# Kernel tuning notes

Measured on AMD Instinct MI355X. Metric: run time of the kernel, lower is better.

The kernel has to match this reference:

```python
import jax, jax.numpy as jnp
import numpy as np

EMB = 1024
HEADS = 16
HEAD_DIM = EMB // HEADS
ROPE_BASE = 10000.0


def rotate_half(x):
    # Interleaved rotate: pairs (x0,x1,x2,x3,...) -> (-x1,x0,-x3,x2,...)
    x1 = x[..., ::2]
    x2 = x[..., 1::2]
    return jnp.stack((-x2, x1), axis=-1).reshape(x.shape)


def rope_cos_sin(seq_len, head_dim):
    inv_freq = 1.0 / (ROPE_BASE ** (jnp.arange(0, head_dim, 2, dtype=jnp.float32) / head_dim))
    pos = jnp.arange(seq_len, dtype=jnp.float32)
    freqs = jnp.outer(pos, inv_freq)            # [S, hd/2]
    emb = jnp.concatenate([freqs, freqs], -1)   # [S, hd]  (NOTE: concat, matching source)
    return jnp.cos(emb)[None, None], jnp.sin(emb)[None, None]  # [1,1,S,hd]


def setup_inputs() -> dict:
    key = jax.random.key(0)
    ks = jax.random.split(key, 5)
    B, S = 2, 2048
    x = jax.random.normal(ks[0], (B, S, EMB), dtype=jnp.float32)
    scale = EMB ** -0.5
    Wq = jax.random.normal(ks[1], (EMB, EMB), dtype=jnp.float32) * scale
    Wk = jax.random.normal(ks[2], (EMB, EMB), dtype=jnp.float32) * scale
    Wv = jax.random.normal(ks[3], (EMB, EMB), dtype=jnp.float32) * scale
    Wo = jax.random.normal(ks[4], (EMB, EMB), dtype=jnp.float32) * scale
    return {"x": x, "Wq": Wq, "Wk": Wk, "Wv": Wv, "Wo": Wo}


def reference(x, Wq, Wk, Wv, Wo):
    B, S, E = x.shape
    def shape_heads(t):
        return t.reshape(B, S, HEADS, HEAD_DIM).transpose(0, 2, 1, 3)  # [B,H,S,hd]
    q = shape_heads(x @ Wq.T)
    k = shape_heads(x @ Wk.T)
    v = shape_heads(x @ Wv.T)
    cos, sin = rope_cos_sin(S, HEAD_DIM)
    q = q * cos + rotate_half(q) * sin
    k = k * cos + rotate_half(k) * sin
    scale = HEAD_DIM ** -0.5
    scores = jnp.einsum('bhqd,bhkd->bhqk', q, k) * scale  # [B,H,S,S]
    causal = jnp.triu(jnp.ones((S, S), dtype=bool), k=1)
    scores = jnp.where(causal, -jnp.inf, scores)
    attn = jax.nn.softmax(scores, axis=-1)
    out = jnp.einsum('bhqk,bhkd->bhqd', attn, v)           # [B,H,S,hd]
    out = out.transpose(0, 2, 1, 3).reshape(B, S, E)
    return out @ Wo.T
```

## Files before the change

### kernel.cpp

```cpp
#include <hip/hip_runtime.h>
#include <cstdint>
#include <cstddef>

typedef __bf16 bf16;
typedef __attribute__((ext_vector_type(8))) __bf16 bf16x8;
typedef __attribute__((ext_vector_type(4))) __bf16 bf16x4;
typedef __attribute__((ext_vector_type(4))) float f32x4;

constexpr int kS = 2048;
constexpr int kH = 16;
constexpr int kD = 64;

__device__ __forceinline__ void gload16(const bf16* g, bf16* l) {
  __builtin_amdgcn_global_load_lds((const __attribute__((address_space(1))) void*)g,
                                   (__attribute__((address_space(3))) void*)l, 16, 0, 0);
}

__global__ __launch_bounds__(256) void cast_all_kernel(
    const float* __restrict__ x, const float* __restrict__ wq, const float* __restrict__ wk,
    const float* __restrict__ wv, const float* __restrict__ wo,
    bf16* __restrict__ xb, bf16* __restrict__ wqb, bf16* __restrict__ wkb,
    bf16* __restrict__ wvb, bf16* __restrict__ wob) {
  int idx = blockIdx.x * 256 + threadIdx.x;
  const float* src; bf16* dst; int i;
  if (idx < (1 << 20)) { src = x; dst = xb; i = idx << 2; }
  else {
    int r = idx - (1 << 20);
    int t = r >> 18;
    i = (r & ((1 << 18) - 1)) << 2;
    src = (t == 0) ? wq : (t == 1) ? wk : (t == 2) ? wv : wo;
    dst = (t == 0) ? wqb : (t == 1) ? wkb : (t == 2) ? wvb : wob;
  }
  float4 v = *(const float4*)(src + i);
  bf16x4 o;
  o[0] = (bf16)v.x; o[1] = (bf16)v.y; o[2] = (bf16)v.z; o[3] = (bf16)v.w;
  *(bf16x4*)(dst + i) = o;
}


#define GSTAGE(BUF, KT)                                    \
  gload16(aP0 + (KT), &As[BUF][(w * 64 + l) * 8]);         \
  gload16(aP1 + (KT), &As[BUF][((4 + w) * 64 + l) * 8]);   \
  gload16(bP0 + (KT), &Bs[BUF][(w * 64 + l) * 8]);         \
  gload16(bP1 + (KT), &Bs[BUF][((4 + w) * 64 + l) * 8]);

__global__ __launch_bounds__(256) void gemm_qkv(const bf16* __restrict__ A,
                                                const bf16* __restrict__ wq,
                                                const bf16* __restrict__ wk,
                                                const bf16* __restrict__ wv,
                                                bf16* __restrict__ qo,
                                                bf16* __restrict__ ko,
                                                bf16* __restrict__ vto) {
  __shared__ bf16 As[2][128 * 32];
  __shared__ bf16 Bs[2][128 * 32];
  const int tid = threadIdx.x;
  const int w = tid >> 6, l = tid & 63;
  const int wr = w >> 1, wc = w & 1;
  const int lr = l & 15, lg = l >> 4;

  const int fid = (blockIdx.x & 7) * 96 + (blockIdx.x >> 3);
  const int mblk = fid & 31;
  const int ntile = fid >> 5;
  const int which = ntile >> 3;
  const int m0 = mblk * 128;
  const int n0 = (ntile & 7) * 128;
  const bf16* Bw = (which == 0) ? wq : (which == 1) ? wk : wv;

  const int srow = l >> 2;
  const int skcol = ((l & 3) ^ ((l >> 3) & 3)) << 3;
  const int K = 1024;

  const bf16* aP0 = A + (size_t)(m0 + w * 16 + srow) * K + skcol;
  const bf16* aP1 = A + (size_t)(m0 + 64 + w * 16 + srow) * K + skcol;
  const bf16* bP0 = Bw + (size_t)(n0 + w * 16 + srow) * K + skcol;
  const bf16* bP1 = Bw + (size_t)(n0 + 64 + w * 16 + srow) * K + skcol;

  f32x4 acc[4][4] = {};
  const int ca = (lg ^ ((lr >> 1) & 3)) * 8;

  GSTAGE(0, 0)
  __syncthreads();
  int cur = 0;
  for (int kt = 0; kt < K; kt += 32) {
    if (kt + 32 < K) { GSTAGE(cur ^ 1, kt + 32) }
    bf16x8 af[4], bfg[4];
#pragma unroll
    for (int mi = 0; mi < 4; mi++)
      af[mi] = *(const bf16x8*)&As[cur][(wr * 64 + mi * 16 + lr) * 32 + ca];
#pragma unroll
    for (int ni = 0; ni < 4; ni++)
      bfg[ni] = *(const bf16x8*)&Bs[cur][(wc * 64 + ni * 16 + lr) * 32 + ca];
    __builtin_amdgcn_s_setprio(1);
#pragma unroll
    for (int mi = 0; mi < 4; mi++)
#pragma unroll
      for (int ni = 0; ni < 4; ni++)
        acc[mi][ni] = __builtin_amdgcn_mfma_f32_16x16x32_bf16(af[mi], bfg[ni], acc[mi][ni], 0, 0, 0);
    __builtin_amdgcn_s_setprio(0);
    __syncthreads();
    cur ^= 1;
  }

  float invf_[4];
#pragma unroll
  for (int ni = 0; ni < 4; ni++) {
    int d31 = ((n0 + wc * 64 + ni * 16 + lr) & 63) & 31;
    invf_[ni] = exp2f((float)d31 * -0.41524100480466348f);
  }

#pragma unroll
  for (int mi = 0; mi < 4; mi++) {
#pragma unroll
    for (int ni = 0; ni < 4; ni++) {
#pragma unroll
      for (int r = 0; r < 4; r++) {
        const int m = m0 + wr * 64 + mi * 16 + lg * 4 + r;
        const int n = n0 + wc * 64 + ni * 16 + lr;
        float v = acc[mi][ni][r];
        const int st = m & 2047;
        const size_t bh = (size_t)(m >> 11) * kH + (n >> 6);
        if (which < 2) {
          float vp = __shfl_xor(v, 1);
          const int d = n & 63;
          float th = (float)st * invf_[ni];
          float sth = __sinf(th), cth = __cosf(th);
          float rv = v * cth + ((d & 1) ? vp : -vp) * sth;
          if (which == 1) rv *= 0.18033688011112042f;
          bf16* dst = which ? ko : qo;
          dst[((bh << 11) + st) * kD + d] = (bf16)rv;
        } else {
          int pos = (st & ~31) | (((st >> 2) & 3) << 3) | (((st >> 4) & 1) << 2) | (st & 3);
          vto[((bh * kD + (n & 63)) << 11) + pos] = (bf16)v;
        }
      }
    }
  }
}

__global__ __launch_bounds__(256) void gemm_out(const bf16* __restrict__ A,
                                                const bf16* __restrict__ Bw,
                                                float* __restrict__ Cout) {
  __shared__ bf16 As[2][128 * 32];
  __shared__ bf16 Bs[2][128 * 32];
  const int tid = threadIdx.x;
  const int w = tid >> 6, l = tid & 63;
  const int wr = w >> 1, wc = w & 1;
  const int lr = l & 15, lg = l >> 4;
  const int m0 = blockIdx.y * 128, n0 = blockIdx.x * 128;
  const int K = 1024, N = 1024;

  const int srow = l >> 2;
  const int skcol = ((l & 3) ^ ((l >> 3) & 3)) << 3;

  const bf16* aP0 = A + (size_t)(m0 + w * 16 + srow) * K + skcol;
  const bf16* aP1 = A + (size_t)(m0 + 64 + w * 16 + srow) * K + skcol;
  const bf16* bP0 = Bw + (size_t)(n0 + w * 16 + srow) * K + skcol;
  const bf16* bP1 = Bw + (size_t)(n0 + 64 + w * 16 + srow) * K + skcol;

  f32x4 acc[4][4] = {};
  const int ca = (lg ^ ((lr >> 1) & 3)) * 8;

  GSTAGE(0, 0)
  __syncthreads();
  int cur = 0;
  for (int kt = 0; kt < K; kt += 32) {
    if (kt + 32 < K) { GSTAGE(cur ^ 1, kt + 32) }
    bf16x8 af[4], bfg[4];
#pragma unroll
    for (int mi = 0; mi < 4; mi++)
      af[mi] = *(const bf16x8*)&As[cur][(wr * 64 + mi * 16 + lr) * 32 + ca];
#pragma unroll
    for (int ni = 0; ni < 4; ni++)
      bfg[ni] = *(const bf16x8*)&Bs[cur][(wc * 64 + ni * 16 + lr) * 32 + ca];
    __builtin_amdgcn_s_setprio(1);
#pragma unroll
    for (int mi = 0; mi < 4; mi++)
#pragma unroll
      for (int ni = 0; ni < 4; ni++)
        acc[mi][ni] = __builtin_amdgcn_mfma_f32_16x16x32_bf16(af[mi], bfg[ni], acc[mi][ni], 0, 0, 0);
    __builtin_amdgcn_s_setprio(0);
    __syncthreads();
    cur ^= 1;
  }

#pragma unroll
  for (int mi = 0; mi < 4; mi++)
#pragma unroll
    for (int ni = 0; ni < 4; ni++)
#pragma unroll
      for (int r = 0; r < 4; r++) {
        const int m = m0 + wr * 64 + mi * 16 + lg * 4 + r;
        const int n = n0 + wc * 64 + ni * 16 + lr;
        Cout[(size_t)m * N + n] = acc[mi][ni][r];
      }
}


#define STAGE(BUF, KV0)                                                                  \
  {                                                                                      \
    _Pragma("unroll") for (int j_ = 0; j_ < 4; j_++) {                                   \
      const int ch_ = w * 4 + j_;                                                        \
      gload16(kh + (size_t)((KV0) + (ch_ >> 1) * 16 + lr) * 64 + (ch_ & 1) * 32 + lg * 8, \
              &Ks[BUF][ch_ * 512 + l * 8]);                                              \
    }                                                                                    \
    _Pragma("unroll") for (int j_ = 0; j_ < 4; j_++) {                                   \
      const int ch_ = w * 4 + j_;                                                        \
      gload16(vh + (size_t)((ch_ >> 2) * 16 + lr) * 2048 + (KV0) + (ch_ & 3) * 32 + lg * 8, \
              &Vs[BUF][ch_ * 512 + l * 8]);                                              \
    }                                                                                    \
  }

#define COMPUTE(BUF, DIAG, O, LPART, QF, QROW, KVB)                                      \
  {                                                                                      \
    bf16x8 kf_[8][2];                                                                    \
    _Pragma("unroll") for (int s_ = 0; s_ < 8; s_++)                                     \
      _Pragma("unroll") for (int c_ = 0; c_ < 2; c_++)                                   \
        kf_[s_][c_] = *(const bf16x8*)&Ks[BUF][(s_ * 2 + c_) * 512 + l * 8];             \
    f32x4 sa_[8] = {};                                                                   \
    __builtin_amdgcn_s_setprio(1);                                                       \
    _Pragma("unroll") for (int s_ = 0; s_ < 8; s_++) {                                   \
      sa_[s_] = __builtin_amdgcn_mfma_f32_16x16x32_bf16(kf_[s_][0], QF[0], sa_[s_], 0, 0, 0); \
      sa_[s_] = __builtin_amdgcn_mfma_f32_16x16x32_bf16(kf_[s_][1], QF[1], sa_[s_], 0, 0, 0); \
    }                                                                                    \
    __builtin_amdgcn_s_setprio(0);                                                       \
    bf16x8 pf_[4];                                                                       \
    float sum0_ = 0.0f, sum1_ = 0.0f;                                                    \
    _Pragma("unroll") for (int s_ = 0; s_ < 8; s_++)                                     \
      _Pragma("unroll") for (int r_ = 0; r_ < 4; r_++) {                                 \
        float sc_ = sa_[s_][r_];                                                         \
        if (DIAG) {                                                                      \
          int kk_ = (KVB) + s_ * 16 + lg * 4 + r_;                                       \
          sc_ = (kk_ <= (QROW)) ? sc_ : -1e30f;                                          \
        }                                                                                \
        float e_ = exp2f(sc_);                                                           \
        if (s_ & 1) sum1_ += e_; else sum0_ += e_;                                       \
        pf_[s_ >> 1][(s_ & 1) * 4 + r_] = (bf16)e_;                                      \
      }                                                                                  \
    LPART += sum0_ + sum1_;                                                              \
    bf16x8 vf_[4][4];                                                                    \
    _Pragma("unroll") for (int c_ = 0; c_ < 4; c_++)                                     \
      _Pragma("unroll") for (int f_ = 0; f_ < 4; f_++)                                   \
        vf_[c_][f_] = *(const bf16x8*)&Vs[BUF][(c_ * 4 + f_) * 512 + l * 8];             \
    __builtin_amdgcn_s_setprio(1);                                                       \
    _Pragma("unroll") for (int c_ = 0; c_ < 4; c_++)                                     \
      _Pragma("unroll") for (int f_ = 0; f_ < 4; f_++)                                   \
        O[c_] = __builtin_amdgcn_mfma_f32_16x16x32_bf16(vf_[c_][f_], pf_[f_], O[c_], 0, 0, 0); \
    __builtin_amdgcn_s_setprio(0);                                                       \
  }

#define EPILOG(O, LPART, Q0)                                                             \
  {                                                                                      \
    float lt_ = LPART;                                                                   \
    lt_ += __shfl_xor(lt_, 16);                                                          \
    lt_ += __shfl_xor(lt_, 32);                                                          \
    const float inv_ = 1.0f / lt_;                                                       \
    _Pragma("unroll") for (int c_ = 0; c_ < 4; c_++) {                                   \
      bf16x4 ov_;                                                                        \
      _Pragma("unroll") for (int r_ = 0; r_ < 4; r_++) ov_[r_] = (bf16)(O[c_][r_] * inv_); \
      size_t addr_ = ((size_t)(b * kS + (Q0) + lr)) * (kH * kD) + h * 64 + c_ * 16 + lg * 4; \
      *(bf16x4*)&ob[addr_] = ov_;                                                        \
    }                                                                                    \
  }

__global__ __launch_bounds__(256, 2) void attn_kernel(const bf16* __restrict__ qb,
                                                      const bf16* __restrict__ kb,
                                                      const bf16* __restrict__ vtb,
                                                      bf16* __restrict__ ob) {
  __shared__ bf16 Ks[2][8192];
  __shared__ bf16 Vs[2][8192];
  const int tid = threadIdx.x;
  const int w = tid >> 6, l = tid & 63;
  const int lr = l & 15, lg = l >> 4;
  const int bid = blockIdx.x;
  const int bh = bid & 31;
  const int qt = 31 - (bid >> 5);
  const bf16* qh = qb + (size_t)bh * (kS * kD);
  const bf16* kh = kb + (size_t)bh * (kS * kD);
  const bf16* vh = vtb + (size_t)bh * (kS * kD);
  const int b = bh >> 4, h = bh & 15;

  const int q0 = qt * 64 + w * 16;
  const int q = q0 + lr;
  bf16x8 qf[2];
#pragma unroll
  for (int c = 0; c < 2; c++)
    qf[c] = *(const bf16x8*)&qh[(size_t)(q0 + lr) * kD + c * 32 + lg * 8];

  float lpart = 0.0f;
  f32x4 o[4] = {};
  const int nkv = (qt + 2) >> 1;

  STAGE(0, 0)
  __syncthreads();
  int cur = 0;
  for (int t = 0; t < nkv; t++) {
    if (t + 1 < nkv) STAGE(cur ^ 1, (t + 1) * 128)
    COMPUTE(cur, (t == nkv - 1), o, lpart, qf, q, t * 128)
    __syncthreads();
    cur ^= 1;
  }
  EPILOG(o, lpart, q0)
}

extern "C" void kernel_launch(void* const* d_in, const int* in_sizes, int n_in,
                              void* d_out, int out_size, void* d_ws, size_t ws_size,
                              hipStream_t stream) {
  const float* x  = (const float*)d_in[0];
  const float* wq = (const float*)d_in[1];
  const float* wk = (const float*)d_in[2];
  const float* wv = (const float*)d_in[3];
  const float* wo = (const float*)d_in[4];

  bf16* xb  = (bf16*)d_ws;
  bf16* qb  = xb + (1 << 22);
  bf16* kb  = qb + (1 << 22);
  bf16* vtb = kb + (1 << 22);
  bf16* ab  = vtb + (1 << 22);
  bf16* wqb = ab + (1 << 22);
  bf16* wkb = wqb + (1 << 20);
  bf16* wvb = wkb + (1 << 20);
  bf16* wob = wvb + (1 << 20);

  cast_all_kernel<<<8192, 256, 0, stream>>>(x, wq, wk, wv, wo, xb, wqb, wkb, wvb, wob);
  gemm_qkv<<<768, 256, 0, stream>>>(xb, wqb, wkb, wvb, qb, kb, vtb);
  attn_kernel<<<1024, 256, 0, stream>>>(qb, kb, vtb, ab);
  gemm_out<<<dim3(8, 32), 256, 0, stream>>>(ab, wob, (float*)d_out);
}
```

Baseline: 127.3 us.

## Retile QKV GEMM to 256x256 blocks with 8 waves and phased prefetch

Rewrites the fused QKV projection GEMM to use 256x256 output tiles with BK=64, 512 threads (8 waves, each computing 128x64), and 192 blocks instead of 768. The main loop is split into four compute phases per K-step, with the next tile's global-to-LDS loads interleaved into the first two phases. Explicit barriers and waitcnts replace the single syncthreads. This aims to raise arithmetic intensity and hide load latency. In exchange it uses about 128KB of LDS at occupancy 1, and 192 blocks may underfill the 256 CUs.

```diff
diff --git a/kernel.cpp b/kernel.cpp
--- a/kernel.cpp
+++ b/kernel.cpp
@@ -37,91 +37,112 @@
   *(bf16x4*)(dst + i) = o;
 }
 
-
-#define GSTAGE(BUF, KT)                                    \
-  gload16(aP0 + (KT), &As[BUF][(w * 64 + l) * 8]);         \
-  gload16(aP1 + (KT), &As[BUF][((4 + w) * 64 + l) * 8]);   \
-  gload16(bP0 + (KT), &Bs[BUF][(w * 64 + l) * 8]);         \
-  gload16(bP1 + (KT), &Bs[BUF][((4 + w) * 64 + l) * 8]);
-
-__global__ __launch_bounds__(256) void gemm_qkv(const bf16* __restrict__ A,
-                                                const bf16* __restrict__ wq,
-                                                const bf16* __restrict__ wk,
-                                                const bf16* __restrict__ wv,
-                                                bf16* __restrict__ qo,
-                                                bf16* __restrict__ ko,
-                                                bf16* __restrict__ vto) {
-  __shared__ bf16 As[2][128 * 32];
-  __shared__ bf16 Bs[2][128 * 32];
+__global__ __launch_bounds__(512, 1) void gemm_qkv(const bf16* __restrict__ A,
+                                                   const bf16* __restrict__ wq,
+                                                   const bf16* __restrict__ wk,
+                                                   const bf16* __restrict__ wv,
+                                                   bf16* __restrict__ qo,
+                                                   bf16* __restrict__ ko,
+                                                   bf16* __restrict__ vto) {
+  __shared__ bf16 As[2][256 * 64];
+  __shared__ bf16 Bs[2][256 * 64];
   const int tid = threadIdx.x;
   const int w = tid >> 6, l = tid & 63;
-  const int wr = w >> 1, wc = w & 1;
+  const int wr = w >> 2, wc = w & 3;
   const int lr = l & 15, lg = l >> 4;
 
-  const int fid = (blockIdx.x & 7) * 96 + (blockIdx.x >> 3);
-  const int mblk = fid & 31;
-  const int ntile = fid >> 5;
-  const int which = ntile >> 3;
-  const int m0 = mblk * 128;
-  const int n0 = (ntile & 7) * 128;
+  const int fid = (blockIdx.x & 7) * 24 + (blockIdx.x >> 3);
+  const int mblk = fid & 15;
+  const int ntile = fid >> 4;
+  const int which = ntile >> 2;
+  const int m0 = mblk * 256;
+  const int n0g = (ntile & 3) * 256;
   const bf16* Bw = (which == 0) ? wq : (which == 1) ? wk : wv;
-
-  const int srow = l >> 2;
-  const int skcol = ((l & 3) ^ ((l >> 3) & 3)) << 3;
   const int K = 1024;
 
-  const bf16* aP0 = A + (size_t)(m0 + w * 16 + srow) * K + skcol;
-  const bf16* aP1 = A + (size_t)(m0 + 64 + w * 16 + srow) * K + skcol;
-  const bf16* bP0 = Bw + (size_t)(n0 + w * 16 + srow) * K + skcol;
-  const bf16* bP1 = Bw + (size_t)(n0 + 64 + w * 16 + srow) * K + skcol;
-
-  f32x4 acc[4][4] = {};
-  const int ca = (lg ^ ((lr >> 1) & 3)) * 8;
-
-  GSTAGE(0, 0)
-  __syncthreads();
+  const int srow8 = l >> 3;
+  const int gslot = (l & 7) ^ srow8;
+  const bf16* aBase = A + (size_t)(m0 + w * 32 + srow8) * K + gslot * 8;
+  const bf16* bBase = Bw + (size_t)(n0g + w * 32 + srow8) * K + gslot * 8;
+
+  f32x4 acc[8][4] = {};
+
+#define ST_A(BUF, J, KT) gload16(aBase + (size_t)(J) * 8 * K + (KT), &As[BUF][(w * 32 + (J) * 8) * 64 + l * 8]);
+#define ST_B(BUF, J, KT) gload16(bBase + (size_t)(J) * 8 * K + (KT), &Bs[BUF][(w * 32 + (J) * 8) * 64 + l * 8]);
+
+#define PHASE(BUF, QM, QN, DO_STAGE, J0, KT1)                                            \
+  {                                                                                      \
+    bf16x8 af_[4][2], bf_[2][2];                                                         \
+    _Pragma("unroll") for (int i_ = 0; i_ < 4; i_++)                                     \
+      _Pragma("unroll") for (int kk_ = 0; kk_ < 2; kk_++) {                              \
+        const int ar_ = wr * 128 + ((QM) * 4 + i_) * 16 + lr;                            \
+        const int sl_ = (kk_ * 4 + lg) ^ (lr & 7);                                       \
+        af_[i_][kk_] = *(const bf16x8*)&As[BUF][ar_ * 64 + sl_ * 8];                     \
+      }                                                                                  \
+    _Pragma("unroll") for (int i_ = 0; i_ < 2; i_++)                                     \
+      _Pragma("unroll") for (int kk_ = 0; kk_ < 2; kk_++) {                              \
+        const int br_ = wc * 64 + ((QN) * 2 + i_) * 16 + lr;                             \
+        const int sl_ = (kk_ * 4 + lg) ^ (lr & 7);                                       \
+        bf_[i_][kk_] = *(const bf16x8*)&Bs[BUF][br_ * 64 + sl_ * 8];                     \
+      }                                                                                  \
+    if (DO_STAGE) {                                                                      \
+      ST_A(BUF ^ 1, (J0), KT1) ST_A(BUF ^ 1, (J0) + 1, KT1)                              \
+      ST_B(BUF ^ 1, (J0), KT1) ST_B(BUF ^ 1, (J0) + 1, KT1)                              \
+    }                                                                                    \
+    __builtin_amdgcn_s_barrier();                                                        \
+    asm volatile("s_waitcnt lgkmcnt(0)" ::: "memory");                                   \
+    __builtin_amdgcn_sched_barrier(0);                                                   \
+    __builtin_amdgcn_s_setprio(1);                                                       \
+    _Pragma("unroll") for (int i_ = 0; i_ < 4; i_++)                                     \
+      _Pragma("unroll") for (int i2_ = 0; i2_ < 2; i2_++)                                \
+        _Pragma("unroll") for (int kk_ = 0; kk_ < 2; kk_++)                              \
+          acc[(QM) * 4 + i_][(QN) * 2 + i2_] = __builtin_amdgcn_mfma_f32_16x16x32_bf16(  \
+              af_[i_][kk_], bf_[i2_][kk_], acc[(QM) * 4 + i_][(QN) * 2 + i2_], 0, 0, 0); \
+    __builtin_amdgcn_s_setprio(0);                                                       \
+  }
+
+#pragma unroll
+  for (int j = 0; j < 4; j++) { ST_A(0, j, 0) ST_B(0, j, 0) }
+  asm volatile("s_waitcnt vmcnt(0)" ::: "memory");
+  __builtin_amdgcn_s_barrier();
+
   int cur = 0;
-  for (int kt = 0; kt < K; kt += 32) {
-    if (kt + 32 < K) { GSTAGE(cur ^ 1, kt + 32) }
-    bf16x8 af[4], bfg[4];
-#pragma unroll
-    for (int mi = 0; mi < 4; mi++)
-      af[mi] = *(const bf16x8*)&As[cur][(wr * 64 + mi * 16 + lr) * 32 + ca];
-#pragma unroll
-    for (int ni = 0; ni < 4; ni++)
-      bfg[ni] = *(const bf16x8*)&Bs[cur][(wc * 64 + ni * 16 + lr) * 32 + ca];
-    __builtin_amdgcn_s_setprio(1);
-#pragma unroll
-    for (int mi = 0; mi < 4; mi++)
-#pragma unroll
-      for (int ni = 0; ni < 4; ni++)
-        acc[mi][ni] = __builtin_amdgcn_mfma_f32_16x16x32_bf16(af[mi], bfg[ni], acc[mi][ni], 0, 0, 0);
-    __builtin_amdgcn_s_setprio(0);
-    __syncthreads();
+  for (int t = 0; t < 16; ++t) {
+    const int kt1 = (t + 1) * 64;
+    const bool stg = (t + 1 < 16);
+    PHASE(cur, 0, 0, stg, 0, kt1)
+    PHASE(cur, 0, 1, stg, 2, kt1)
+    PHASE(cur, 1, 0, false, 0, 0)
+    PHASE(cur, 1, 1, false, 0, 0)
+    asm volatile("s_waitcnt vmcnt(0)" ::: "memory");
+    __builtin_amdgcn_s_barrier();
     cur ^= 1;
   }
+#undef PHASE
+#undef ST_A
+#undef ST_B
 
   float invf_[4];
 #pragma unroll
   for (int ni = 0; ni < 4; ni++) {
-    int d31 = ((n0 + wc * 64 + ni * 16 + lr) & 63) & 31;
+    int d31 = (ni * 16 + lr) & 31;
     invf_[ni] = exp2f((float)d31 * -0.41524100480466348f);
   }
 
 #pragma unroll
-  for (int mi = 0; mi < 4; mi++) {
+  for (int mi = 0; mi < 8; mi++) {
 #pragma unroll
     for (int ni = 0; ni < 4; ni++) {
 #pragma unroll
       for (int r = 0; r < 4; r++) {
-        const int m = m0 + wr * 64 + mi * 16 + lg * 4 + r;
-        const int n = n0 + wc * 64 + ni * 16 + lr;
+        const int m = m0 + wr * 128 + mi * 16 + lg * 4 + r;
+        const int nt = n0g + wc * 64 + ni * 16 + lr;
         float v = acc[mi][ni][r];
         const int st = m & 2047;
-        const size_t bh = (size_t)(m >> 11) * kH + (n >> 6);
+        const size_t bh = (size_t)(m >> 11) * kH + (nt >> 6);
         if (which < 2) {
           float vp = __shfl_xor(v, 1);
-          const int d = n & 63;
+          const int d = nt & 63;
           float th = (float)st * invf_[ni];
           float sth = __sinf(th), cth = __cosf(th);
           float rv = v * cth + ((d & 1) ? vp : -vp) * sth;
@@ -130,12 +151,18 @@
           dst[((bh << 11) + st) * kD + d] = (bf16)rv;
         } else {
           int pos = (st & ~31) | (((st >> 2) & 3) << 3) | (((st >> 4) & 1) << 2) | (st & 3);
-          vto[((bh * kD + (n & 63)) << 11) + pos] = (bf16)v;
+          vto[((bh * kD + (nt & 63)) << 11) + pos] = (bf16)v;
         }
       }
     }
   }
 }
+
+#define GSTAGE(BUF, KT)                                    \
+  gload16(aP0 + (KT), &As[BUF][(w * 64 + l) * 8]);         \
+  gload16(aP1 + (KT), &As[BUF][((4 + w) * 64 + l) * 8]);   \
+  gload16(bP0 + (KT), &Bs[BUF][(w * 64 + l) * 8]);         \
+  gload16(bP1 + (KT), &Bs[BUF][((4 + w) * 64 + l) * 8]);
 
 __global__ __launch_bounds__(256) void gemm_out(const bf16* __restrict__ A,
                                                 const bf16* __restrict__ Bw,
@@ -194,7 +221,6 @@
         Cout[(size_t)m * N + n] = acc[mi][ni][r];
       }
 }
-
 
 #define STAGE(BUF, KV0)                                                                  \
   {                                                                                      \
@@ -322,7 +348,7 @@
   bf16* wob = wvb + (1 << 20);
 
   cast_all_kernel<<<8192, 256, 0, stream>>>(x, wq, wk, wv, wo, xb, wqb, wkb, wvb, wob);
-  gemm_qkv<<<768, 256, 0, stream>>>(xb, wqb, wkb, wvb, qb, kb, vtb);
+  gemm_qkv<<<192, 512, 0, stream>>>(xb, wqb, wkb, wvb, qb, kb, vtb);
   attn_kernel<<<1024, 256, 0, stream>>>(qb, kb, vtb, ab);
   gemm_out<<<dim3(8, 32), 256, 0, stream>>>(ab, wob, (float*)d_out);
 }
```

Measured after the change: 139.2 us. 1.09x slower.

## Triple-buffer GEMM K-loop with vmcnt-based waits and a single barrier per step

Applied to the files above, without the earlier changes.

Both the QKV and output projection GEMMs switch from double to triple-buffered LDS staging. Each step waits only for the oldest tile's global-to-LDS loads with a partial s_waitcnt vmcnt, then hits one barrier before issuing the next prefetch two tiles ahead. The aim is to hide global load latency better and drop the extra full barrier per iteration. In exchange LDS use per block grows to 48KB, which may reduce occupancy.

```diff
diff --git a/kernel.cpp b/kernel.cpp
--- a/kernel.cpp
+++ b/kernel.cpp
@@ -38,11 +38,46 @@
 }
 
 
-#define GSTAGE(BUF, KT)                                    \
-  gload16(aP0 + (KT), &As[BUF][(w * 64 + l) * 8]);         \
-  gload16(aP1 + (KT), &As[BUF][((4 + w) * 64 + l) * 8]);   \
-  gload16(bP0 + (KT), &Bs[BUF][(w * 64 + l) * 8]);         \
+#define GSTAGE3(BUF, KT)                                    \
+  gload16(aP0 + (KT), &As[BUF][(w * 64 + l) * 8]);          \
+  gload16(aP1 + (KT), &As[BUF][((4 + w) * 64 + l) * 8]);    \
+  gload16(bP0 + (KT), &Bs[BUF][(w * 64 + l) * 8]);          \
   gload16(bP1 + (KT), &Bs[BUF][((4 + w) * 64 + l) * 8]);
+
+#define GCOMPUTE(BUF)                                                                \
+  {                                                                                  \
+    bf16x8 af[4], bfg[4];                                                            \
+    _Pragma("unroll") for (int mi = 0; mi < 4; mi++)                                 \
+      af[mi] = *(const bf16x8*)&As[BUF][(wr * 64 + mi * 16 + lr) * 32 + ca];         \
+    _Pragma("unroll") for (int ni = 0; ni < 4; ni++)                                 \
+      bfg[ni] = *(const bf16x8*)&Bs[BUF][(wc * 64 + ni * 16 + lr) * 32 + ca];        \
+    __builtin_amdgcn_s_setprio(1);                                                   \
+    _Pragma("unroll") for (int mi = 0; mi < 4; mi++)                                 \
+      _Pragma("unroll") for (int ni = 0; ni < 4; ni++)                               \
+        acc[mi][ni] = __builtin_amdgcn_mfma_f32_16x16x32_bf16(af[mi], bfg[ni], acc[mi][ni], 0, 0, 0); \
+    __builtin_amdgcn_s_setprio(0);                                                   \
+  }
+
+#define GBODY(BUF, NXT, T, DOSTG)                                                    \
+  asm volatile("s_waitcnt vmcnt(4)" ::: "memory");                                   \
+  __builtin_amdgcn_s_barrier();                                                      \
+  if (DOSTG) { GSTAGE3(NXT, ((T) + 2) * 32) }                                        \
+  GCOMPUTE(BUF)
+
+#define GEMM_KLOOP3                                                                  \
+  GSTAGE3(0, 0)                                                                      \
+  GSTAGE3(1, 32)                                                                     \
+  for (int t = 0; t < 30; t += 3) {                                                  \
+    GBODY(0, 2, t, true)                                                             \
+    GBODY(1, 0, t + 1, true)                                                         \
+    GBODY(2, 1, t + 2, true)                                                         \
+  }                                                                                  \
+  asm volatile("s_waitcnt vmcnt(4)" ::: "memory");                                   \
+  __builtin_amdgcn_s_barrier();                                                      \
+  GCOMPUTE(0)                                                                        \
+  asm volatile("s_waitcnt vmcnt(0)" ::: "memory");                                   \
+  __builtin_amdgcn_s_barrier();                                                      \
+  GCOMPUTE(1)
 
 __global__ __launch_bounds__(256) void gemm_qkv(const bf16* __restrict__ A,
                                                 const bf16* __restrict__ wq,
@@ -51,8 +86,8 @@
                                                 bf16* __restrict__ qo,
                                                 bf16* __restrict__ ko,
                                                 bf16* __restrict__ vto) {
-  __shared__ bf16 As[2][128 * 32];
-  __shared__ bf16 Bs[2][128 * 32];
+  __shared__ bf16 As[3][128 * 32];
+  __shared__ bf16 Bs[3][128 * 32];
   const int tid = threadIdx.x;
   const int w = tid >> 6, l = tid & 63;
   const int wr = w >> 1, wc = w & 1;
@@ -78,28 +113,7 @@
   f32x4 acc[4][4] = {};
   const int ca = (lg ^ ((lr >> 1) & 3)) * 8;
 
-  GSTAGE(0, 0)
-  __syncthreads();
-  int cur = 0;
-  for (int kt = 0; kt < K; kt += 32) {
-    if (kt + 32 < K) { GSTAGE(cur ^ 1, kt + 32) }
-    bf16x8 af[4], bfg[4];
-#pragma unroll
-    for (int mi = 0; mi < 4; mi++)
-      af[mi] = *(const bf16x8*)&As[cur][(wr * 64 + mi * 16 + lr) * 32 + ca];
-#pragma unroll
-    for (int ni = 0; ni < 4; ni++)
-      bfg[ni] = *(const bf16x8*)&Bs[cur][(wc * 64 + ni * 16 + lr) * 32 + ca];
-    __builtin_amdgcn_s_setprio(1);
-#pragma unroll
-    for (int mi = 0; mi < 4; mi++)
-#pragma unroll
-      for (int ni = 0; ni < 4; ni++)
-        acc[mi][ni] = __builtin_amdgcn_mfma_f32_16x16x32_bf16(af[mi], bfg[ni], acc[mi][ni], 0, 0, 0);
-    __builtin_amdgcn_s_setprio(0);
-    __syncthreads();
-    cur ^= 1;
-  }
+  GEMM_KLOOP3
 
   float invf_[4];
 #pragma unroll
@@ -140,8 +154,8 @@
 __global__ __launch_bounds__(256) void gemm_out(const bf16* __restrict__ A,
                                                 const bf16* __restrict__ Bw,
                                                 float* __restrict__ Cout) {
-  __shared__ bf16 As[2][128 * 32];
-  __shared__ bf16 Bs[2][128 * 32];
+  __shared__ bf16 As[3][128 * 32];
+  __shared__ bf16 Bs[3][128 * 32];
   const int tid = threadIdx.x;
   const int w = tid >> 6, l = tid & 63;
   const int wr = w >> 1, wc = w & 1;
@@ -160,28 +174,7 @@
   f32x4 acc[4][4] = {};
   const int ca = (lg ^ ((lr >> 1) & 3)) * 8;
 
-  GSTAGE(0, 0)
-  __syncthreads();
-  int cur = 0;
-  for (int kt = 0; kt < K; kt += 32) {
-    if (kt + 32 < K) { GSTAGE(cur ^ 1, kt + 32) }
-    bf16x8 af[4], bfg[4];
-#pragma unroll
-    for (int mi = 0; mi < 4; mi++)
-      af[mi] = *(const bf16x8*)&As[cur][(wr * 64 + mi * 16 + lr) * 32 + ca];
-#pragma unroll
-    for (int ni = 0; ni < 4; ni++)
-      bfg[ni] = *(const bf16x8*)&Bs[cur][(wc * 64 + ni * 16 + lr) * 32 + ca];
-    __builtin_amdgcn_s_setprio(1);
-#pragma unroll
-    for (int mi = 0; mi < 4; mi++)
-#pragma unroll
-      for (int ni = 0; ni < 4; ni++)
-        acc[mi][ni] = __builtin_amdgcn_mfma_f32_16x16x32_bf16(af[mi], bfg[ni], acc[mi][ni], 0, 0, 0);
-    __builtin_amdgcn_s_setprio(0);
-    __syncthreads();
-    cur ^= 1;
-  }
+  GEMM_KLOOP3
 
 #pragma unroll
   for (int mi = 0; mi < 4; mi++)
@@ -194,7 +187,6 @@
         Cout[(size_t)m * N + n] = acc[mi][ni][r];
       }
 }
-
 
 #define STAGE(BUF, KV0)                                                                  \
   {                                                                                      \
```

Result: slower. 145.0 us (+13.9%).
